# Kernel optimization log

Hardware: AMD Instinct MI355X
Metric: run time of the kernel (lower is better)

Reference implementation:

```python
import jax, jax.numpy as jnp
import numpy as np

NBINS = 256


def setup_inputs() -> dict:
    key = jax.random.key(0)
    x = jax.random.uniform(key, (16, 3, 1024, 1024), dtype=jnp.float32)
    return {"x": x}


def reference(x):
    b, c, h, w = x.shape
    n = b * c
    xf = x.reshape(n, h * w)                      # (n, N) per-channel rows

    # global min/max over the whole tensor (matches torch.histogram range)
    mn = xf.min()
    mx = xf.max()
    span = mx - mn

    # per-row histogram via scatter-add; last bin is right-closed like torch.histogram
    scale = NBINS / span
    idx = jnp.clip(jnp.floor((xf - mn) * scale).astype(jnp.int32), 0, NBINS - 1)
    flat_idx = (jnp.arange(n, dtype=jnp.int32)[:, None] * NBINS + idx).reshape(-1)
    hist = jax.ops.segment_sum(
        jnp.ones((n * h * w,), dtype=jnp.float32), flat_idx,
        num_segments=n * NBINS,
    ).reshape(n, NBINS)
    hist = hist / hist.sum(axis=1, keepdims=True)  # normalized histograms

    # vectorized Otsu: cumulative weights/means -> inter-class variance
    t = jnp.arange(NBINS, dtype=hist.dtype)
    w_bg = jnp.cumsum(hist, axis=1)               # background weight up to t
    s_bg = jnp.cumsum(hist * t, axis=1)           # background weighted sum
    total = s_bg[:, -1:]                          # sum_i i*hist[i]
    w_fg = 1.0 - w_bg
    valid = (w_bg > 0) & (w_fg > 0)
    mean_bg = s_bg / jnp.where(w_bg > 0, w_bg, 1.0)
    mean_fg = (total - s_bg) / jnpp_safe(w_fg) if False else (total - s_bg) / jnp.where(w_fg > 0, w_fg, 1.0)
    var = jnp.where(valid, w_bg * w_fg * (mean_bg - mean_fg) ** 2, -jnp.inf)
    t_opt = jnp.argmax(var, axis=1)               # first max, like strict `>` loop

    # threshold = right edge of the optimal bin
    edges = mn + span * (jnp.arange(NBINS + 1, dtype=x.dtype) / NBINS)
    thresh = edges[t_opt + 1]                     # (n,)

    out = jnp.where(xf <= thresh[:, None], jnp.zeros((), x.dtype), xf)
    return out.reshape(b, c, h, w)
```

## Files before the change

### kernel.cpp

```cpp
#include <hip/hip_runtime.h>
#include <stdint.h>

#define NBINS 256
#define HW_SHIFT 20
#define HW4_SHIFT (HW_SHIFT-2)
#define BLK_PER_IMG 32
#define NCOPY 32
#define MM_BLOCKS 1024

typedef float nfloat4 __attribute__((ext_vector_type(4)));

__device__ __forceinline__ unsigned enc_f(float f) {
    unsigned u = __float_as_uint(f);
    return u ^ ((unsigned)((int)u >> 31) | 0x80000000u);
}
__device__ __forceinline__ float dec_f(unsigned e) {
    unsigned u = (e & 0x80000000u) ? (e ^ 0x80000000u) : ~e;
    return __uint_as_float(u);
}


__global__ void k_minmax(const float4* __restrict__ x, unsigned* __restrict__ bmm, long n4) {
    unsigned mn = 0xFFFFFFFFu, mx = 0u;
    long stride = (long)gridDim.x * blockDim.x;
    for (long i = (long)blockIdx.x * blockDim.x + threadIdx.x; i < n4; i += stride) {
        float4 v = x[i];
        unsigned e0 = enc_f(v.x), e1 = enc_f(v.y), e2 = enc_f(v.z), e3 = enc_f(v.w);
        mn = min(mn, min(min(e0, e1), min(e2, e3)));
        mx = max(mx, max(max(e0, e1), max(e2, e3)));
    }
    for (int off = 32; off > 0; off >>= 1) {
        mn = min(mn, (unsigned)__shfl_down((int)mn, off));
        mx = max(mx, (unsigned)__shfl_down((int)mx, off));
    }
    __shared__ unsigned smn[4], smx[4];
    int lane = threadIdx.x & 63, w = threadIdx.x >> 6;
    if (lane == 0) { smn[w] = mn; smx[w] = mx; }
    __syncthreads();
    if (threadIdx.x == 0) {
        for (int j = 1; j < (int)(blockDim.x >> 6); j++) {
            mn = min(mn, smn[j]); mx = max(mx, smx[j]);
        }
        bmm[2 * blockIdx.x]     = mn;
        bmm[2 * blockIdx.x + 1] = mx;
    }
}

__global__ void k_reduce(const unsigned* __restrict__ bmm, unsigned* __restrict__ mmo) {
    unsigned mn = 0xFFFFFFFFu, mx = 0u;
    for (int i = threadIdx.x; i < MM_BLOCKS; i += blockDim.x) {
        mn = min(mn, bmm[2 * i]);
        mx = max(mx, bmm[2 * i + 1]);
    }
    for (int off = 32; off > 0; off >>= 1) {
        mn = min(mn, (unsigned)__shfl_down((int)mn, off));
        mx = max(mx, (unsigned)__shfl_down((int)mx, off));
    }
    __shared__ unsigned smn[4], smx[4];
    int lane = threadIdx.x & 63, w = threadIdx.x >> 6;
    if (lane == 0) { smn[w] = mn; smx[w] = mx; }
    __syncthreads();
    if (threadIdx.x == 0) {
        for (int j = 1; j < (int)(blockDim.x >> 6); j++) {
            mn = min(mn, smn[j]); mx = max(mx, smx[j]);
        }
        mmo[0] = mn; mmo[1] = mx;
    }
}

__global__ void k_hist(const float4* __restrict__ x, const unsigned* __restrict__ mmo,
                       unsigned* __restrict__ partial) {
    __shared__ unsigned sh[NBINS * NCOPY];
    for (int i = threadIdx.x; i < NBINS * NCOPY; i += blockDim.x) sh[i] = 0u;
    __syncthreads();
    float mn = dec_f(mmo[0]);
    float mx = dec_f(mmo[1]);
    float span = mx - mn;
    float scale = __fdiv_rn(256.0f, span);
    int img = blockIdx.x / BLK_PER_IMG;
    int blk = blockIdx.x % BLK_PER_IMG;
    const int chunk = (1 << HW4_SHIFT) / BLK_PER_IMG;
    const float4* base = x + ((long)img << HW4_SHIFT) + (long)blk * chunk;
    int c = threadIdx.x & (NCOPY - 1);
    for (int i = threadIdx.x; i < chunk; i += blockDim.x) {
        float4 v = base[i];
        int b0 = (int)floorf((v.x - mn) * scale);
        int b1 = (int)floorf((v.y - mn) * scale);
        int b2 = (int)floorf((v.z - mn) * scale);
        int b3 = (int)floorf((v.w - mn) * scale);
        b0 = min(max(b0, 0), NBINS - 1);
        b1 = min(max(b1, 0), NBINS - 1);
        b2 = min(max(b2, 0), NBINS - 1);
        b3 = min(max(b3, 0), NBINS - 1);
        atomicAdd(&sh[b0 * NCOPY + c], 1u);
        atomicAdd(&sh[b1 * NCOPY + c], 1u);
        atomicAdd(&sh[b2 * NCOPY + c], 1u);
        atomicAdd(&sh[b3 * NCOPY + c], 1u);
    }
    __syncthreads();
    int bin = threadIdx.x;
    unsigned sum = 0;
    #pragma unroll
    for (int k = 0; k < NCOPY; k++) {
        int cc = (k + threadIdx.x) & (NCOPY - 1);
        sum += sh[bin * NCOPY + cc];
    }
    partial[(long)blockIdx.x * NBINS + bin] = sum;
}

__global__ void k_otsu(const unsigned* __restrict__ partial, const unsigned* __restrict__ mmo,
                       float* __restrict__ thresh) {
    __shared__ unsigned h[NBINS];
    int img = blockIdx.x;
    int bin = threadIdx.x;
    const unsigned* p = partial + (long)img * BLK_PER_IMG * NBINS;
    unsigned sum = 0;
    #pragma unroll
    for (int k = 0; k < BLK_PER_IMG; k++) sum += p[k * NBINS + bin];
    h[bin] = sum;
    __syncthreads();
    if (threadIdx.x != 0) return;
    const float inv_total = 1.0f / 1048576.0f;
    float w = 0.0f, s = 0.0f;
    for (int t = 0; t < NBINS; t++) {
        float pp = __fmul_rn((float)h[t], inv_total);
        w = __fadd_rn(w, pp);
        s = __fadd_rn(s, __fmul_rn(pp, (float)t));
    }
    float total = s;
    float best = -__builtin_inff();
    int bestt = 0;
    w = 0.0f; s = 0.0f;
    for (int t = 0; t < NBINS; t++) {
        float pp = __fmul_rn((float)h[t], inv_total);
        w = __fadd_rn(w, pp);
        s = __fadd_rn(s, __fmul_rn(pp, (float)t));
        float wf = __fsub_rn(1.0f, w);
        float var;
        if (w > 0.0f && wf > 0.0f) {
            float mb = __fdiv_rn(s, w);
            float mf = __fdiv_rn(__fsub_rn(total, s), wf);
            float d = __fsub_rn(mb, mf);
            var = __fmul_rn(__fmul_rn(w, wf), __fmul_rn(d, d));
        } else {
            var = -__builtin_inff();
        }
        if (var > best) { best = var; bestt = t; }
    }
    float mn = dec_f(mmo[0]);
    float mx = dec_f(mmo[1]);
    float span = __fsub_rn(mx, mn);
    float q = __fmul_rn((float)(bestt + 1), 1.0f / 256.0f);
    thresh[img] = __fadd_rn(mn, __fmul_rn(span, q));
}

__global__ void k_apply(const float4* __restrict__ x, nfloat4* __restrict__ out,
                        const float* __restrict__ thresh, long n4) {
    long stride = (long)gridDim.x * blockDim.x;
    for (long i = (long)blockIdx.x * blockDim.x + threadIdx.x; i < n4; i += stride) {
        int img = (int)(i >> HW4_SHIFT);
        float th = thresh[img];
        float4 v = x[i];
        nfloat4 o;
        o.x = (v.x <= th) ? 0.0f : v.x;
        o.y = (v.y <= th) ? 0.0f : v.y;
        o.z = (v.z <= th) ? 0.0f : v.z;
        o.w = (v.w <= th) ? 0.0f : v.w;
        __builtin_nontemporal_store(o, &out[i]);
    }
}

extern "C" void kernel_launch(void* const* d_in, const int* in_sizes, int n_in,
                              void* d_out, int out_size, void* d_ws, size_t ws_size,
                              hipStream_t stream) {
    const float* x = (const float*)d_in[0];
    float* out = (float*)d_out;
    long n = (long)in_sizes[0];
    long n4 = n >> 2;
    int nimg = (int)(n >> HW_SHIFT);

    unsigned* bmm = (unsigned*)d_ws;
    unsigned* mmo = bmm + 2 * MM_BLOCKS;
    unsigned* partial = mmo + 2;
    float* thresh = (float*)(partial + (long)nimg * BLK_PER_IMG * NBINS);

    k_minmax<<<MM_BLOCKS, 256, 0, stream>>>((const float4*)x, bmm, n4);
    k_reduce<<<1, 256, 0, stream>>>(bmm, mmo);
    k_hist<<<nimg * BLK_PER_IMG, 256, 0, stream>>>((const float4*)x, mmo, partial);
    k_otsu<<<nimg, 256, 0, stream>>>(partial, mmo, thresh);
    k_apply<<<4096, 256, 0, stream>>>((const float4*)x, (nfloat4*)out, thresh, n4);
}
```

Measured before the change: 438.5 us.

## Fuse all Otsu stages into one cooperative persistent kernel with grid syncs

Replaces the five-kernel pipeline (minmax, reduce, histogram, otsu, apply) with one cooperative kernel of 768 blocks. The stages are separated by grid.sync, which removes the launch gaps and the tiny single-block kernels. The Otsu argmax is also parallelised across 256 threads using a packed key reduction instead of a serial loop on one thread. The cost is three grid-wide barriers, a fixed grid that has to be co-resident, and occupancy limited by 32KB of shared memory per block.

```diff
diff --git a/kernel.cpp b/kernel.cpp
--- a/kernel.cpp
+++ b/kernel.cpp
@@ -1,12 +1,17 @@
 #include <hip/hip_runtime.h>
+#include <hip/hip_cooperative_groups.h>
 #include <stdint.h>
+
+namespace cg = cooperative_groups;
 
 #define NBINS 256
 #define HW_SHIFT 20
-#define HW4_SHIFT (HW_SHIFT-2)
-#define BLK_PER_IMG 32
+#define HW4_SHIFT 18
+#define GRID 768
+#define BLOCK 256
 #define NCOPY 32
-#define MM_BLOCKS 1024
+#define CHUNKS_PER_IMG 32
+#define CHUNK4 8192
 
 typedef float nfloat4 __attribute__((ext_vector_type(4)));
 
@@ -14,179 +19,234 @@
     unsigned u = __float_as_uint(f);
     return u ^ ((unsigned)((int)u >> 31) | 0x80000000u);
 }
-__device__ __forceinline__ float dec_f(unsigned e) {
-    unsigned u = (e & 0x80000000u) ? (e ^ 0x80000000u) : ~e;
-    return __uint_as_float(u);
-}
-
-
-__global__ void k_minmax(const float4* __restrict__ x, unsigned* __restrict__ bmm, long n4) {
-    unsigned mn = 0xFFFFFFFFu, mx = 0u;
-    long stride = (long)gridDim.x * blockDim.x;
-    for (long i = (long)blockIdx.x * blockDim.x + threadIdx.x; i < n4; i += stride) {
-        float4 v = x[i];
-        unsigned e0 = enc_f(v.x), e1 = enc_f(v.y), e2 = enc_f(v.z), e3 = enc_f(v.w);
-        mn = min(mn, min(min(e0, e1), min(e2, e3)));
-        mx = max(mx, max(max(e0, e1), max(e2, e3)));
-    }
-    for (int off = 32; off > 0; off >>= 1) {
-        mn = min(mn, (unsigned)__shfl_down((int)mn, off));
-        mx = max(mx, (unsigned)__shfl_down((int)mx, off));
-    }
-    __shared__ unsigned smn[4], smx[4];
-    int lane = threadIdx.x & 63, w = threadIdx.x >> 6;
-    if (lane == 0) { smn[w] = mn; smx[w] = mx; }
-    __syncthreads();
-    if (threadIdx.x == 0) {
-        for (int j = 1; j < (int)(blockDim.x >> 6); j++) {
-            mn = min(mn, smn[j]); mx = max(mx, smx[j]);
-        }
-        bmm[2 * blockIdx.x]     = mn;
-        bmm[2 * blockIdx.x + 1] = mx;
-    }
-}
-
-__global__ void k_reduce(const unsigned* __restrict__ bmm, unsigned* __restrict__ mmo) {
-    unsigned mn = 0xFFFFFFFFu, mx = 0u;
-    for (int i = threadIdx.x; i < MM_BLOCKS; i += blockDim.x) {
-        mn = min(mn, bmm[2 * i]);
-        mx = max(mx, bmm[2 * i + 1]);
-    }
-    for (int off = 32; off > 0; off >>= 1) {
-        mn = min(mn, (unsigned)__shfl_down((int)mn, off));
-        mx = max(mx, (unsigned)__shfl_down((int)mx, off));
-    }
-    __shared__ unsigned smn[4], smx[4];
-    int lane = threadIdx.x & 63, w = threadIdx.x >> 6;
-    if (lane == 0) { smn[w] = mn; smx[w] = mx; }
-    __syncthreads();
-    if (threadIdx.x == 0) {
-        for (int j = 1; j < (int)(blockDim.x >> 6); j++) {
-            mn = min(mn, smn[j]); mx = max(mx, smx[j]);
-        }
-        mmo[0] = mn; mmo[1] = mx;
-    }
-}
-
-__global__ void k_hist(const float4* __restrict__ x, const unsigned* __restrict__ mmo,
-                       unsigned* __restrict__ partial) {
+
+
+__global__ void __launch_bounds__(BLOCK, 3)
+k_fused_otsu(const float4* __restrict__ x, nfloat4* __restrict__ out,
+             float* __restrict__ ws, int nimg) {
+    cg::grid_group grid = cg::this_grid();
     __shared__ unsigned sh[NBINS * NCOPY];
-    for (int i = threadIdx.x; i < NBINS * NCOPY; i += blockDim.x) sh[i] = 0u;
-    __syncthreads();
-    float mn = dec_f(mmo[0]);
-    float mx = dec_f(mmo[1]);
+
+    const int tid = threadIdx.x;
+    const int bid = blockIdx.x;
+    const int lane = tid & 63;
+    const int wv = tid >> 6;
+    const long n4 = (long)nimg << HW4_SHIFT;
+    const long stride = (long)GRID * BLOCK;
+
+    float2* bmm = (float2*)ws;
+    unsigned* partial = (unsigned*)(ws + 2 * GRID);
+    float* thresh = ws + 2 * GRID + (long)nimg * CHUNKS_PER_IMG * NBINS;
+
+    float mn = __builtin_inff(), mx = -__builtin_inff();
+    {
+        long i = (long)bid * BLOCK + tid;
+        for (; i + 3 * stride < n4; i += 4 * stride) {
+            float4 a = x[i];
+            float4 b = x[i + stride];
+            float4 c4 = x[i + 2 * stride];
+            float4 d = x[i + 3 * stride];
+            mn = fminf(mn, fminf(fminf(a.x, a.y), fminf(a.z, a.w)));
+            mx = fmaxf(mx, fmaxf(fmaxf(a.x, a.y), fmaxf(a.z, a.w)));
+            mn = fminf(mn, fminf(fminf(b.x, b.y), fminf(b.z, b.w)));
+            mx = fmaxf(mx, fmaxf(fmaxf(b.x, b.y), fmaxf(b.z, b.w)));
+            mn = fminf(mn, fminf(fminf(c4.x, c4.y), fminf(c4.z, c4.w)));
+            mx = fmaxf(mx, fmaxf(fmaxf(c4.x, c4.y), fmaxf(c4.z, c4.w)));
+            mn = fminf(mn, fminf(fminf(d.x, d.y), fminf(d.z, d.w)));
+            mx = fmaxf(mx, fmaxf(fmaxf(d.x, d.y), fmaxf(d.z, d.w)));
+        }
+        for (; i < n4; i += stride) {
+            float4 a = x[i];
+            mn = fminf(mn, fminf(fminf(a.x, a.y), fminf(a.z, a.w)));
+            mx = fmaxf(mx, fmaxf(fmaxf(a.x, a.y), fmaxf(a.z, a.w)));
+        }
+    }
+    for (int off = 32; off; off >>= 1) {
+        mn = fminf(mn, __shfl_down(mn, off));
+        mx = fmaxf(mx, __shfl_down(mx, off));
+    }
+    if (lane == 0) { sh[2 * wv] = __float_as_uint(mn); sh[2 * wv + 1] = __float_as_uint(mx); }
+    __syncthreads();
+    if (tid == 0) {
+        for (int j = 1; j < BLOCK / 64; j++) {
+            mn = fminf(mn, __uint_as_float(sh[2 * j]));
+            mx = fmaxf(mx, __uint_as_float(sh[2 * j + 1]));
+        }
+        bmm[bid] = make_float2(mn, mx);
+    }
+    __threadfence();
+    grid.sync();
+
+    mn = __builtin_inff(); mx = -__builtin_inff();
+    for (int j = tid; j < GRID; j += BLOCK) {
+        float2 v = bmm[j];
+        mn = fminf(mn, v.x); mx = fmaxf(mx, v.y);
+    }
+    for (int off = 32; off; off >>= 1) {
+        mn = fminf(mn, __shfl_down(mn, off));
+        mx = fmaxf(mx, __shfl_down(mx, off));
+    }
+    if (lane == 0) { sh[2 * wv] = __float_as_uint(mn); sh[2 * wv + 1] = __float_as_uint(mx); }
+    __syncthreads();
+    if (tid == 0) {
+        for (int j = 1; j < BLOCK / 64; j++) {
+            mn = fminf(mn, __uint_as_float(sh[2 * j]));
+            mx = fmaxf(mx, __uint_as_float(sh[2 * j + 1]));
+        }
+        sh[0] = __float_as_uint(mn); sh[1] = __float_as_uint(mx);
+    }
+    __syncthreads();
+    mn = __uint_as_float(sh[0]);
+    mx = __uint_as_float(sh[1]);
     float span = mx - mn;
     float scale = __fdiv_rn(256.0f, span);
-    int img = blockIdx.x / BLK_PER_IMG;
-    int blk = blockIdx.x % BLK_PER_IMG;
-    const int chunk = (1 << HW4_SHIFT) / BLK_PER_IMG;
-    const float4* base = x + ((long)img << HW4_SHIFT) + (long)blk * chunk;
-    int c = threadIdx.x & (NCOPY - 1);
-    for (int i = threadIdx.x; i < chunk; i += blockDim.x) {
-        float4 v = base[i];
-        int b0 = (int)floorf((v.x - mn) * scale);
-        int b1 = (int)floorf((v.y - mn) * scale);
-        int b2 = (int)floorf((v.z - mn) * scale);
-        int b3 = (int)floorf((v.w - mn) * scale);
-        b0 = min(max(b0, 0), NBINS - 1);
-        b1 = min(max(b1, 0), NBINS - 1);
-        b2 = min(max(b2, 0), NBINS - 1);
-        b3 = min(max(b3, 0), NBINS - 1);
-        atomicAdd(&sh[b0 * NCOPY + c], 1u);
-        atomicAdd(&sh[b1 * NCOPY + c], 1u);
-        atomicAdd(&sh[b2 * NCOPY + c], 1u);
-        atomicAdd(&sh[b3 * NCOPY + c], 1u);
-    }
-    __syncthreads();
-    int bin = threadIdx.x;
-    unsigned sum = 0;
-    #pragma unroll
-    for (int k = 0; k < NCOPY; k++) {
-        int cc = (k + threadIdx.x) & (NCOPY - 1);
-        sum += sh[bin * NCOPY + cc];
-    }
-    partial[(long)blockIdx.x * NBINS + bin] = sum;
-}
-
-__global__ void k_otsu(const unsigned* __restrict__ partial, const unsigned* __restrict__ mmo,
-                       float* __restrict__ thresh) {
-    __shared__ unsigned h[NBINS];
-    int img = blockIdx.x;
-    int bin = threadIdx.x;
-    const unsigned* p = partial + (long)img * BLK_PER_IMG * NBINS;
-    unsigned sum = 0;
-    #pragma unroll
-    for (int k = 0; k < BLK_PER_IMG; k++) sum += p[k * NBINS + bin];
-    h[bin] = sum;
-    __syncthreads();
-    if (threadIdx.x != 0) return;
-    const float inv_total = 1.0f / 1048576.0f;
-    float w = 0.0f, s = 0.0f;
-    for (int t = 0; t < NBINS; t++) {
-        float pp = __fmul_rn((float)h[t], inv_total);
-        w = __fadd_rn(w, pp);
-        s = __fadd_rn(s, __fmul_rn(pp, (float)t));
-    }
-    float total = s;
-    float best = -__builtin_inff();
-    int bestt = 0;
-    w = 0.0f; s = 0.0f;
-    for (int t = 0; t < NBINS; t++) {
-        float pp = __fmul_rn((float)h[t], inv_total);
-        w = __fadd_rn(w, pp);
-        s = __fadd_rn(s, __fmul_rn(pp, (float)t));
-        float wf = __fsub_rn(1.0f, w);
+
+    const int nchunks = nimg * CHUNKS_PER_IMG;
+    const int c = tid & (NCOPY - 1);
+    for (int chunk = bid; chunk < nchunks; chunk += GRID) {
+        __syncthreads();
+        for (int i = tid; i < NBINS * NCOPY; i += BLOCK) sh[i] = 0u;
+        __syncthreads();
+        const float4* base = x + ((long)(chunk >> 5) << HW4_SHIFT)
+                               + (long)(chunk & (CHUNKS_PER_IMG - 1)) * CHUNK4;
+        for (int i = tid; i < CHUNK4; i += 2 * BLOCK) {
+            float4 v0 = base[i];
+            float4 v1 = base[i + BLOCK];
+            int b0 = (int)floorf((v0.x - mn) * scale);
+            int b1 = (int)floorf((v0.y - mn) * scale);
+            int b2 = (int)floorf((v0.z - mn) * scale);
+            int b3 = (int)floorf((v0.w - mn) * scale);
+            int b4 = (int)floorf((v1.x - mn) * scale);
+            int b5 = (int)floorf((v1.y - mn) * scale);
+            int b6 = (int)floorf((v1.z - mn) * scale);
+            int b7 = (int)floorf((v1.w - mn) * scale);
+            b0 = min(max(b0, 0), NBINS - 1); b1 = min(max(b1, 0), NBINS - 1);
+            b2 = min(max(b2, 0), NBINS - 1); b3 = min(max(b3, 0), NBINS - 1);
+            b4 = min(max(b4, 0), NBINS - 1); b5 = min(max(b5, 0), NBINS - 1);
+            b6 = min(max(b6, 0), NBINS - 1); b7 = min(max(b7, 0), NBINS - 1);
+            atomicAdd(&sh[b0 * NCOPY + c], 1u);
+            atomicAdd(&sh[b1 * NCOPY + c], 1u);
+            atomicAdd(&sh[b2 * NCOPY + c], 1u);
+            atomicAdd(&sh[b3 * NCOPY + c], 1u);
+            atomicAdd(&sh[b4 * NCOPY + c], 1u);
+            atomicAdd(&sh[b5 * NCOPY + c], 1u);
+            atomicAdd(&sh[b6 * NCOPY + c], 1u);
+            atomicAdd(&sh[b7 * NCOPY + c], 1u);
+        }
+        __syncthreads();
+        unsigned sum = 0;
+        #pragma unroll
+        for (int k = 0; k < NCOPY; k++) {
+            int cc = (k + tid) & (NCOPY - 1);
+            sum += sh[tid * NCOPY + cc];
+        }
+        partial[(long)chunk * NBINS + tid] = sum;
+    }
+    __threadfence();
+    grid.sync();
+
+    if (bid < nimg) {
+        const unsigned* p = partial + (long)bid * CHUNKS_PER_IMG * NBINS;
+        unsigned hsum = 0;
+        #pragma unroll 4
+        for (int k = 0; k < CHUNKS_PER_IMG; k++) hsum += p[k * NBINS + tid];
+        sh[tid] = hsum;
+        __syncthreads();
+        if (tid == 0) {
+            const float inv_total = 1.0f / 1048576.0f;
+            float ww = 0.0f, ss = 0.0f;
+            for (int t = 0; t < NBINS; t++) {
+                float pp = __fmul_rn((float)sh[t], inv_total);
+                ww = __fadd_rn(ww, pp);
+                ss = __fadd_rn(ss, __fmul_rn(pp, (float)t));
+                sh[NBINS + t] = __float_as_uint(ww);
+                sh[2 * NBINS + t] = __float_as_uint(ss);
+            }
+        }
+        __syncthreads();
+        float total = __uint_as_float(sh[3 * NBINS - 1]);
+        float ww = __uint_as_float(sh[NBINS + tid]);
+        float ss = __uint_as_float(sh[2 * NBINS + tid]);
+        float wf = __fsub_rn(1.0f, ww);
         float var;
-        if (w > 0.0f && wf > 0.0f) {
-            float mb = __fdiv_rn(s, w);
-            float mf = __fdiv_rn(__fsub_rn(total, s), wf);
+        if (ww > 0.0f && wf > 0.0f) {
+            float mb = __fdiv_rn(ss, ww);
+            float mf = __fdiv_rn(__fsub_rn(total, ss), wf);
             float d = __fsub_rn(mb, mf);
-            var = __fmul_rn(__fmul_rn(w, wf), __fmul_rn(d, d));
+            var = __fmul_rn(__fmul_rn(ww, wf), __fmul_rn(d, d));
         } else {
             var = -__builtin_inff();
         }
-        if (var > best) { best = var; bestt = t; }
-    }
-    float mn = dec_f(mmo[0]);
-    float mx = dec_f(mmo[1]);
-    float span = __fsub_rn(mx, mn);
-    float q = __fmul_rn((float)(bestt + 1), 1.0f / 256.0f);
-    thresh[img] = __fadd_rn(mn, __fmul_rn(span, q));
-}
-
-__global__ void k_apply(const float4* __restrict__ x, nfloat4* __restrict__ out,
-                        const float* __restrict__ thresh, long n4) {
-    long stride = (long)gridDim.x * blockDim.x;
-    for (long i = (long)blockIdx.x * blockDim.x + threadIdx.x; i < n4; i += stride) {
-        int img = (int)(i >> HW4_SHIFT);
-        float th = thresh[img];
-        float4 v = x[i];
-        nfloat4 o;
-        o.x = (v.x <= th) ? 0.0f : v.x;
-        o.y = (v.y <= th) ? 0.0f : v.y;
-        o.z = (v.z <= th) ? 0.0f : v.z;
-        o.w = (v.w <= th) ? 0.0f : v.w;
-        __builtin_nontemporal_store(o, &out[i]);
+        unsigned long long key = ((unsigned long long)enc_f(var) << 32)
+                               | (unsigned)(NBINS - 1 - tid);
+        for (int off = 32; off; off >>= 1) {
+            unsigned long long o = __shfl_down(key, off);
+            key = key > o ? key : o;
+        }
+        if (lane == 0) {
+            sh[3 * NBINS + 2 * wv] = (unsigned)(key & 0xFFFFFFFFull);
+            sh[3 * NBINS + 2 * wv + 1] = (unsigned)(key >> 32);
+        }
+        __syncthreads();
+        if (tid == 0) {
+            for (int j = 1; j < BLOCK / 64; j++) {
+                unsigned long long o = ((unsigned long long)sh[3 * NBINS + 2 * j + 1] << 32)
+                                     | sh[3 * NBINS + 2 * j];
+                key = key > o ? key : o;
+            }
+            int bestt = NBINS - 1 - (int)(key & 0xFFFFFFFFull);
+            float sp = __fsub_rn(mx, mn);
+            float q = __fmul_rn((float)(bestt + 1), 1.0f / 256.0f);
+            thresh[bid] = __fadd_rn(mn, __fmul_rn(sp, q));
+        }
+    }
+    __threadfence();
+    grid.sync();
+
+    if (tid < nimg) sh[tid] = __float_as_uint(thresh[tid]);
+    __syncthreads();
+    {
+        long i = (long)bid * BLOCK + tid;
+        for (; i + stride < n4; i += 2 * stride) {
+            float4 v0 = x[i];
+            float4 v1 = x[i + stride];
+            float t0 = __uint_as_float(sh[(int)(i >> HW4_SHIFT)]);
+            float t1 = __uint_as_float(sh[(int)((i + stride) >> HW4_SHIFT)]);
+            nfloat4 o0, o1;
+            o0.x = (v0.x <= t0) ? 0.0f : v0.x;
+            o0.y = (v0.y <= t0) ? 0.0f : v0.y;
+            o0.z = (v0.z <= t0) ? 0.0f : v0.z;
+            o0.w = (v0.w <= t0) ? 0.0f : v0.w;
+            o1.x = (v1.x <= t1) ? 0.0f : v1.x;
+            o1.y = (v1.y <= t1) ? 0.0f : v1.y;
+            o1.z = (v1.z <= t1) ? 0.0f : v1.z;
+            o1.w = (v1.w <= t1) ? 0.0f : v1.w;
+            __builtin_nontemporal_store(o0, &out[i]);
+            __builtin_nontemporal_store(o1, &out[i + stride]);
+        }
+        for (; i < n4; i += stride) {
+            float4 v0 = x[i];
+            float t0 = __uint_as_float(sh[(int)(i >> HW4_SHIFT)]);
+            nfloat4 o0;
+            o0.x = (v0.x <= t0) ? 0.0f : v0.x;
+            o0.y = (v0.y <= t0) ? 0.0f : v0.y;
+            o0.z = (v0.z <= t0) ? 0.0f : v0.z;
+            o0.w = (v0.w <= t0) ? 0.0f : v0.w;
+            __builtin_nontemporal_store(o0, &out[i]);
+        }
     }
 }
 
 extern "C" void kernel_launch(void* const* d_in, const int* in_sizes, int n_in,
                               void* d_out, int out_size, void* d_ws, size_t ws_size,
                               hipStream_t stream) {
-    const float* x = (const float*)d_in[0];
-    float* out = (float*)d_out;
+    const float4* x = (const float4*)d_in[0];
+    nfloat4* out = (nfloat4*)d_out;
     long n = (long)in_sizes[0];
-    long n4 = n >> 2;
     int nimg = (int)(n >> HW_SHIFT);
-
-    unsigned* bmm = (unsigned*)d_ws;
-    unsigned* mmo = bmm + 2 * MM_BLOCKS;
-    unsigned* partial = mmo + 2;
-    float* thresh = (float*)(partial + (long)nimg * BLK_PER_IMG * NBINS);
-
-    k_minmax<<<MM_BLOCKS, 256, 0, stream>>>((const float4*)x, bmm, n4);
-    k_reduce<<<1, 256, 0, stream>>>(bmm, mmo);
-    k_hist<<<nimg * BLK_PER_IMG, 256, 0, stream>>>((const float4*)x, mmo, partial);
-    k_otsu<<<nimg, 256, 0, stream>>>(partial, mmo, thresh);
-    k_apply<<<4096, 256, 0, stream>>>((const float4*)x, (nfloat4*)out, thresh, n4);
+    float* ws = (float*)d_ws;
+
+    void* args[] = { (void*)&x, (void*)&out, (void*)&ws, (void*)&nimg };
+    hipLaunchCooperativeKernel((const void*)k_fused_otsu, dim3(GRID), dim3(BLOCK),
+                               args, 0, stream);
 }
```

Result: slower. 792.7 us (+80.8%).
